# Kernel optimization log

Measured on AMD Instinct MI355X. Metric: run time of the kernel, lower is better.

Reference implementation:

```python
import jax, jax.numpy as jnp
import numpy as np

M, LAM, MAX_ITER, TOL, BETA = 5, 1e-4, 50, 0.01, 1.0


def anderson_fixed_point(lin_w, lin_b, x0):
    """Anderson acceleration for x = Linear(x), faithful to the torch loop.
    x0: (bsz, d, H, W); the fixed-point map applies the linear over W."""
    bsz = x0.shape[0]
    n = x0.size // bsz
    shape = x0.shape
    dt = x0.dtype

    def f(v_flat):  # (bsz, n) -> (bsz, n)
        return (v_flat.reshape(shape) @ lin_w.T + lin_b).reshape(bsz, n)

    x0f = x0.reshape(bsz, n)
    F0 = f(x0f)
    X = jnp.zeros((bsz, M, n), dt).at[:, 0].set(x0f).at[:, 1].set(F0)
    Fm = jnp.zeros((bsz, M, n), dt).at[:, 0].set(F0).at[:, 1].set(f(F0))
    y = jnp.zeros((bsz, M + 1), dt).at[:, 0].set(1.0)
    eyeM = jnp.eye(M, dtype=dt)

    def cond(c):
        _, _, k, res = c
        return (k < MAX_ITER) & (res >= TOL)

    def body(c):
        X, Fm, k, _ = c
        nk = jnp.minimum(k, M)
        # mask inactive history slots (k < M early iterations); padded rows/cols
        # get lam on the diagonal and 0 border -> alpha_j = 0 there, identical
        # to torch's solve on the leading (n+1)x(n+1) submatrix.
        mask = (jnp.arange(M) < nk).astype(dt)               # (M,)
        G = (Fm - X) * mask[None, :, None]                   # (bsz, M, n)
        Hin = jnp.einsum('bin,bjn->bij', G, G) + LAM * eyeM  # (bsz, M, M)
        H = jnp.zeros((bsz, M + 1, M + 1), dt)
        H = H.at[:, 0, 1:].set(mask).at[:, 1:, 0].set(mask).at[:, 1:, 1:].set(Hin)
        alpha = jnp.linalg.solve(H, y[..., None])[:, 1:, 0]  # (bsz, M)
        xnew = BETA * jnp.einsum('bm,bmn->bn', alpha, Fm) + (1.0 - BETA) * jnp.einsum('bm,bmn->bn', alpha, X)
        idx = k % M
        X = X.at[:, idx].set(xnew)
        fnew = f(xnew)
        Fm = Fm.at[:, idx].set(fnew)
        res = jnp.linalg.norm(fnew - xnew) / (1e-5 + jnp.linalg.norm(fnew))
        return (X, Fm, k + 1, res)

    Xf, _, kf, _ = jax.lax.while_loop(
        cond, body, (X, Fm, jnp.int32(2), jnp.asarray(jnp.inf, dt)))
    return Xf[:, (kf - 1) % M].reshape(shape)


def setup_inputs() -> dict:
    key = jax.random.key(0)
    k1, k2, k3, k4, k5 = jax.random.split(key, 5)
    B, D, H, W = 16, 8, 128, 512  # in_features = out_features = W = 512
    x = jax.random.normal(k1, (B, D, H, W), jnp.float32)
    # contractive inner linear so the fixed-point iteration behaves
    lin_w = jax.random.normal(k2, (W, W), jnp.float32) * 0.02
    lin_b = jax.random.normal(k3, (W,), jnp.float32) * 0.1
    weight = jax.random.normal(k4, (W, W), jnp.float32) * 0.02
    bias = jax.random.normal(k5, (W,), jnp.float32) * 0.1
    return {"x": x, "lin_w": lin_w, "lin_b": lin_b, "weight": weight, "bias": bias}


def reference(x, lin_w, lin_b, weight, bias):
    # torch runs the solver under no_grad -> stop_gradient for fidelity
    x_star = anderson_fixed_point(
        jax.lax.stop_gradient(lin_w),
        jax.lax.stop_gradient(lin_b),
        jax.lax.stop_gradient(x))
    return x_star @ weight.T + bias
```

## Files before the change

### kernel.cpp

```cpp
#include <hip/hip_runtime.h>
#include <math.h>

#define FD     512
#define NBATCH 16
#define NROWS  16384
#define ROWS   64
#define NBLK   (NROWS/ROWS)
#define TPB    1024
#define MM     5
#define LAMV   1e-4f
#define MAXIT  50
#define TOLV   0.01f
#define NTOT   8388608
#define PADW   520

typedef __attribute__((ext_vector_type(8))) short  short8;
typedef __attribute__((ext_vector_type(4))) short  short4v;
typedef __attribute__((ext_vector_type(4))) float  float4v;

__device__ unsigned short g_Fm[MM][NTOT];
__device__ unsigned short g_G [MM][NTOT];
__device__ unsigned short g_Wb [FD*FD];
__device__ unsigned short g_WbO[FD*FD];
__device__ float g_acc [MAXIT-2][NBATCH][8];
__device__ float g_acc0[NBATCH][8];
__device__ float g_alpha[8];
__device__ int   g_lastk;

static __device__ __forceinline__ unsigned short f2bf(float f) {
    unsigned u = __float_as_uint(f);
    u += 0x7fff + ((u >> 16) & 1);
    return (unsigned short)(u >> 16);
}
static __device__ __forceinline__ float bf2f(unsigned short s) {
    return __uint_as_float(((unsigned)s) << 16);
}

template<int MODE>
static __device__ __forceinline__ void mfma_gemm(const unsigned short* __restrict__ Wb,
                                                 const float* __restrict__ bvec,
                                                 const unsigned short* AsIn,
                                                 unsigned short* FsOut,
                                                 float* __restrict__ gout)
{
    const int lane = threadIdx.x & 63;
    const int wv   = threadIdx.x >> 6;
    const int lm   = lane & 15;
    const int quad = lane >> 4;
    float4v acc[4][2];
#pragma unroll
    for (int ct = 0; ct < 2; ct++) {
        const int c0 = wv*32 + ct*16 + quad*4;
#pragma unroll
        for (int r = 0; r < 4; r++) {
            const float b = bvec[c0 + r];
#pragma unroll
            for (int r16 = 0; r16 < 4; r16++) acc[r16][ct][r] = b;
        }
    }
#pragma unroll
    for (int q = 0; q < 4; q++) {
#pragma unroll
        for (int kb = 0; kb < 4; kb++) {
            const int ko = q*128 + kb*32 + quad*8;
            short8 bf[2];
#pragma unroll
            for (int ct = 0; ct < 2; ct++)
                bf[ct] = *(const short8*)(Wb + (wv*32 + ct*16 + lm)*FD + ko);
            short8 af[4];
#pragma unroll
            for (int r16 = 0; r16 < 4; r16++)
                af[r16] = *(const short8*)(AsIn + (r16*16 + lm)*PADW + ko);
#pragma unroll
            for (int r16 = 0; r16 < 4; r16++) {
                acc[r16][0] = __builtin_amdgcn_mfma_f32_16x16x32_bf16(bf[0], af[r16], acc[r16][0], 0,0,0);
                acc[r16][1] = __builtin_amdgcn_mfma_f32_16x16x32_bf16(bf[1], af[r16], acc[r16][1], 0,0,0);
            }
        }
    }
#pragma unroll
    for (int ct = 0; ct < 2; ct++) {
        const int c0 = wv*32 + ct*16 + quad*4;
#pragma unroll
        for (int r16 = 0; r16 < 4; r16++) {
            const int row = r16*16 + lm;
            if (MODE == 0) {
                short4v v;
#pragma unroll
                for (int r = 0; r < 4; r++) v[r] = (short)f2bf(acc[r16][ct][r]);
                *(short4v*)(FsOut + row*PADW + c0) = v;
            } else {
                float4 v;
                v.x = acc[r16][ct][0]; v.y = acc[r16][ct][1];
                v.z = acc[r16][ct][2]; v.w = acc[r16][ct][3];
                *(float4*)(gout + row*FD + c0) = v;
            }
        }
    }
}

static __device__ __forceinline__ void red6(const float vals[6], float (*redS)[8], float* accrow)
{
    const int lane = threadIdx.x & 63, wv = threadIdx.x >> 6;
#pragma unroll
    for (int j = 0; j < 6; j++) {
        float v = vals[j];
#pragma unroll
        for (int o = 32; o; o >>= 1) v += __shfl_down(v, o);
        if (lane == 0) redS[wv][j] = v;
    }
    __syncthreads();
    if (threadIdx.x < 6) {
        float s = 0.f;
#pragma unroll
        for (int w = 0; w < 16; w++) s += redS[w][threadIdx.x];
        atomicAdd(accrow + threadIdx.x, s);
    }
}

__global__ void __launch_bounds__(256) k_init0(const float* __restrict__ lin_w,
                                               const float* __restrict__ weight)
{
    const int i0 = blockIdx.x*256 + threadIdx.x, stride = gridDim.x*256;
    for (int i = i0; i < FD*FD; i += stride) {
        g_Wb [i] = f2bf(lin_w[i]);
        g_WbO[i] = f2bf(weight[i]);
    }
    float* a = &g_acc[0][0][0];
    for (int i = i0; i < (MAXIT-2)*NBATCH*8; i += stride) a[i] = 0.f;
    float* a0 = &g_acc0[0][0];
    for (int i = i0; i < NBATCH*8; i += stride) a0[i] = 0.f;
}

__global__ void __launch_bounds__(TPB, 4) k_init1(const float* __restrict__ x,
                                                  const float* __restrict__ lin_b)
{
    __shared__ __align__(16) unsigned short As[ROWS*PADW];
    __shared__ __align__(16) unsigned short Fs[ROWS*PADW];
    __shared__ float redS[16][8];
    const int tid = threadIdx.x;
    const int t = blockIdx.x, b = t >> 4;
    const int base = t * (ROWS*FD);

#pragma unroll
    for (int i = 0; i < 4; i++) {
        const int e = (i*TPB + tid) * 8;
        const float4 a0 = *(const float4*)(x + base + e);
        const float4 a1 = *(const float4*)(x + base + e + 4);
        short8 v;
        v[0]=f2bf(a0.x); v[1]=f2bf(a0.y); v[2]=f2bf(a0.z); v[3]=f2bf(a0.w);
        v[4]=f2bf(a1.x); v[5]=f2bf(a1.y); v[6]=f2bf(a1.z); v[7]=f2bf(a1.w);
        *(short8*)(As + (e>>9)*PADW + (e&511)) = v;
    }
    __syncthreads();
    mfma_gemm<0>(g_Wb, lin_b, As, Fs, nullptr);
    __syncthreads();
    float d00 = 0.f;
#pragma unroll
    for (int i = 0; i < 4; i++) {
        const int e = (i*TPB + tid) * 8;
        const int off = base + e, lo = (e>>9)*PADW + (e&511);
        const short8 fv = *(const short8*)(Fs + lo);
        const short8 xv = *(const short8*)(As + lo);
        short8 gv;
#pragma unroll
        for (int j = 0; j < 8; j++) {
            const float g = bf2f((unsigned short)fv[j]) - bf2f((unsigned short)xv[j]);
            gv[j] = (short)f2bf(g);
            d00 = fmaf(g, g, d00);
        }
        *(short8*)(&g_Fm[0][off]) = fv;
        *(short8*)(&g_G [0][off]) = gv;
    }
    __syncthreads();
    mfma_gemm<0>(g_Wb, lin_b, Fs, As, nullptr);
    __syncthreads();
    float d01 = 0.f, d11 = 0.f;
#pragma unroll
    for (int i = 0; i < 4; i++) {
        const int e = (i*TPB + tid) * 8;
        const int off = base + e, lo = (e>>9)*PADW + (e&511);
        const short8 f1 = *(const short8*)(As + lo);
        const short8 f0 = *(const short8*)(Fs + lo);
        const short8 g0 = *(const short8*)(&g_G[0][off]);
        short8 gv;
#pragma unroll
        for (int j = 0; j < 8; j++) {
            const float g = bf2f((unsigned short)f1[j]) - bf2f((unsigned short)f0[j]);
            gv[j] = (short)f2bf(g);
            d11 = fmaf(g, g, d11);
            d01 = fmaf(bf2f((unsigned short)g0[j]), g, d01);
        }
        *(short8*)(&g_Fm[1][off]) = f1;
        *(short8*)(&g_G [1][off]) = gv;
    }
    const float vals[6] = {d00, d01, d11, 0.f, 0.f, 0.f};
    red6(vals, redS, &g_acc0[b][0]);
}

__global__ void __launch_bounds__(TPB, 4) k_iter(const float* __restrict__ lin_b, int k)
{
    __shared__ __align__(16) unsigned short As[ROWS*PADW];
    __shared__ __align__(16) unsigned short Fs[ROWS*PADW];
    __shared__ float gramS[MM][MM];
    __shared__ float alphaS[MM];
    __shared__ float Hs[48];
    __shared__ float redS[16][8];
    __shared__ float gAs[MM][MM];
    __shared__ float ga0S[3];
    __shared__ float sres;

    const int tid = threadIdx.x;
    const int t = blockIdx.x, b = t >> 4;
    const int base = t * (ROWS*FD);
    const int it = k - 2, idx = k % MM, nk = (k < MM) ? k : MM;
    const int j0 = (k - 5 > 2) ? (k - 5) : 2;

    if (k > 2 && (tid >> 6) == 0) {
        float v = 0.f;
        if (tid < 32) {
            const int bb = tid & 15;
            const int jj = (tid < 16) ? ((k-1) % MM) : 5;
            v = g_acc[it-1][bb][jj];
        }
        v += __shfl_xor(v, 1); v += __shfl_xor(v, 2);
        v += __shfl_xor(v, 4); v += __shfl_xor(v, 8);
        const float num = __shfl(v, 0), den = __shfl(v, 16);
        if (tid == 0) sres = sqrtf(num) / (1e-5f + sqrtf(den));
    }
    if ((tid >> 6) == 1) {
        const int l = tid & 63;
        if (l < 25) {
            const int jj = j0 + l/5;
            if (jj < k) gAs[l/5][l%5] = g_acc[jj-2][b][l%5];
        } else if (l < 28) {
            ga0S[l-25] = g_acc0[b][l-25];
        }
    }
    __syncthreads();
    if (k > 2 && sres < TOLV) return;

    short8 pf0[MM], pf1[MM];
#pragma unroll
    for (int m = 0; m < MM; m++) if (m < nk) {
        pf0[m] = *(const short8*)(&g_Fm[m][base + (0*TPB + tid)*8]);
        pf1[m] = *(const short8*)(&g_Fm[m][base + (1*TPB + tid)*8]);
    }
    __builtin_amdgcn_sched_barrier(0);

    if (tid == 0) {
#pragma unroll
        for (int i = 0; i < MM; i++)
#pragma unroll
            for (int j = 0; j < MM; j++) gramS[i][j] = 0.f;
        gramS[0][0] = ga0S[0];
        gramS[0][1] = gramS[1][0] = ga0S[1];
        gramS[1][1] = ga0S[2];
        for (int j = j0; j < k; j++) {
            const int ij = j % MM, nkj = (j < MM) ? j : MM;
            for (int c = 0; c < MM; c++)
                if (c < nkj || c == ij) {
                    const float vv = gAs[j - j0][c];
                    gramS[ij][c] = vv; gramS[c][ij] = vv;
                }
        }
        float* H = Hs;
        for (int i = 0; i < 42; i++) H[i] = 0.f;
        for (int j = 0; j < nk; j++) { H[1+j] = 1.f; H[(1+j)*7] = 1.f; }
#pragma unroll
        for (int i = 0; i < MM; i++) H[(1+i)*7 + (1+i)] = LAMV;
        for (int i = 0; i < nk; i++)
            for (int j = 0; j < nk; j++)
                H[(1+i)*7 + (1+j)] = gramS[i][j] + (i == j ? LAMV : 0.f);
        H[6] = 1.f;
        for (int col = 0; col < 6; col++) {
            int p = col; float mx = fabsf(H[col*7+col]);
            for (int r2 = col+1; r2 < 6; r2++) {
                const float vv = fabsf(H[r2*7+col]);
                if (vv > mx) { mx = vv; p = r2; }
            }
            if (p != col)
                for (int j = col; j < 7; j++) { const float tt = H[col*7+j]; H[col*7+j] = H[p*7+j]; H[p*7+j] = tt; }
            const float piv = H[col*7+col];
            for (int r2 = col+1; r2 < 6; r2++) {
                const float fct = H[r2*7+col] / piv;
                for (int j = col+1; j < 7; j++) H[r2*7+j] -= fct * H[col*7+j];
            }
        }
        for (int r2 = 5; r2 >= 0; r2--) {
            float s = H[r2*7+6];
            for (int j = r2+1; j < 6; j++) s -= H[r2*7+j] * H[j*7+6];
            H[r2*7+6] = s / H[r2*7+r2];
        }
#pragma unroll
        for (int m = 0; m < MM; m++) alphaS[m] = H[(1+m)*7+6];
        if (t == 0) {
#pragma unroll
            for (int m = 0; m < MM; m++) g_alpha[m] = H[(1+m)*7+6];
            g_lastk = k;
        }
    }
    __syncthreads();

    float al[MM];
#pragma unroll
    for (int m = 0; m < MM; m++) al[m] = alphaS[m];

#pragma unroll
    for (int i = 0; i < 4; i++) {
        const int e = (i*TPB + tid) * 8;
        const int off = base + e;
        float s[8] = {0,0,0,0,0,0,0,0};
#pragma unroll
        for (int m = 0; m < MM; m++) if (m < nk) {
            short8 fm;
            if (i == 0)      fm = pf0[m];
            else if (i == 1) fm = pf1[m];
            else             fm = *(const short8*)(&g_Fm[m][off]);
#pragma unroll
            for (int j = 0; j < 8; j++)
                s[j] = fmaf(al[m], bf2f((unsigned short)fm[j]), s[j]);
        }
        short8 v;
#pragma unroll
        for (int j = 0; j < 8; j++) v[j] = (short)f2bf(s[j]);
        *(short8*)(As + (e>>9)*PADW + (e&511)) = v;
    }
    __syncthreads();
    mfma_gemm<0>(g_Wb, lin_b, As, Fs, nullptr);
    __syncthreads();
    float dv[6] = {0,0,0,0,0,0};
    float dself = 0.f;
#pragma unroll
    for (int i = 0; i < 4; i++) {
        const int e = (i*TPB + tid) * 8;
        const int off = base + e, lo = (e>>9)*PADW + (e&511);
        const short8 fv = *(const short8*)(Fs + lo);
        const short8 xv = *(const short8*)(As + lo);
        float gg[8]; short8 gv;
#pragma unroll
        for (int j = 0; j < 8; j++) {
            const float ff = bf2f((unsigned short)fv[j]);
            const float g  = ff - bf2f((unsigned short)xv[j]);
            gg[j] = g; gv[j] = (short)f2bf(g);
            dv[5] = fmaf(ff, ff, dv[5]);
            dself = fmaf(g, g, dself);
        }
        *(short8*)(&g_Fm[idx][off]) = fv;
        *(short8*)(&g_G [idx][off]) = gv;
#pragma unroll
        for (int js = 0; js < MM; js++) {
            if (js != idx && js < nk) {
                const short8 gj = *(const short8*)(&g_G[js][off]);
#pragma unroll
                for (int j = 0; j < 8; j++)
                    dv[js] = fmaf(gg[j], bf2f((unsigned short)gj[j]), dv[js]);
            }
        }
    }
    float vals[6];
#pragma unroll
    for (int j = 0; j < MM; j++) vals[j] = (j == idx) ? (dv[j] + dself) : dv[j];
    vals[5] = dv[5];
    red6(vals, redS, &g_acc[it][b][0]);
}

__global__ void __launch_bounds__(TPB, 4) k_final(const float* __restrict__ bias,
                                                  float* __restrict__ out)
{
    __shared__ __align__(16) unsigned short As[ROWS*PADW];
    __shared__ float alphaS[MM];
    __shared__ int   nkS;
    const int tid = threadIdx.x;
    const int base = blockIdx.x * (ROWS*FD);

    if (tid == 0) {
        const int lk = g_lastk;
        nkS = (lk < MM) ? lk : MM;
#pragma unroll
        for (int m = 0; m < MM; m++) alphaS[m] = g_alpha[m];
    }
    __syncthreads();
    const int nk = nkS;
    float al[MM];
#pragma unroll
    for (int m = 0; m < MM; m++) al[m] = alphaS[m];

#pragma unroll
    for (int i = 0; i < 4; i++) {
        const int e = (i*TPB + tid) * 8;
        const int off = base + e;
        float s[8] = {0,0,0,0,0,0,0,0};
#pragma unroll
        for (int m = 0; m < MM; m++) if (m < nk) {
            const short8 fm = *(const short8*)(&g_Fm[m][off]);
#pragma unroll
            for (int j = 0; j < 8; j++)
                s[j] = fmaf(al[m], bf2f((unsigned short)fm[j]), s[j]);
        }
        short8 v;
#pragma unroll
        for (int j = 0; j < 8; j++) v[j] = (short)f2bf(s[j]);
        *(short8*)(As + (e>>9)*PADW + (e&511)) = v;
    }
    __syncthreads();
    mfma_gemm<1>(g_WbO, bias, As, nullptr, out + base);
}

extern "C" void kernel_launch(void* const* d_in, const int* in_sizes, int n_in,
                              void* d_out, int out_size, void* d_ws, size_t ws_size,
                              hipStream_t stream)
{
    (void)in_sizes; (void)n_in; (void)out_size; (void)d_ws; (void)ws_size;
    const float* x      = (const float*)d_in[0];
    const float* lin_w  = (const float*)d_in[1];
    const float* lin_b  = (const float*)d_in[2];
    const float* weight = (const float*)d_in[3];
    const float* bias   = (const float*)d_in[4];
    float* out = (float*)d_out;

    hipLaunchKernelGGL(k_init0, dim3(512),  dim3(256), 0, stream, lin_w, weight);
    hipLaunchKernelGGL(k_init1, dim3(NBLK), dim3(TPB), 0, stream, x, lin_b);
    for (int k = 2; k < MAXIT; k++)
        hipLaunchKernelGGL(k_iter, dim3(NBLK), dim3(TPB), 0, stream, lin_b, k);
    hipLaunchKernelGGL(k_final, dim3(NBLK), dim3(TPB), 0, stream, bias, out);
}
```

Before: 630.7 us.

## Halve rows per block, compute GEMM in place in one LDS buffer

Each block now handles 32 rows instead of 64, so the grid doubles. The separate Fs shared buffer is dropped: the MFMA GEMM writes its result back into As between two barriers, and the x and F values are kept in registers. The early-exit residual check is now done by every wave with no shared variable or barrier. The Fm prefetch before the alpha solve is removed, and k_init1 recomputes G0 rather than re-reading it. Together this cuts LDS use per block, aiming for higher occupancy (launch bounds raised to 8), at the cost of more blocks each re-reading the whole weight matrix and extra barriers inside the GEMM.

Result: slower. 764.5 us (+21.2%).

```diff
diff --git a/kernel.cpp b/kernel.cpp
--- a/kernel.cpp
+++ b/kernel.cpp
@@ -4,9 +4,10 @@
 #define FD     512
 #define NBATCH 16
 #define NROWS  16384
-#define ROWS   64
+#define ROWS   32
 #define NBLK   (NROWS/ROWS)
 #define TPB    1024
+#define BPB    32
 #define MM     5
 #define LAMV   1e-4f
 #define MAXIT  50
@@ -37,17 +38,16 @@
 }
 
 template<int MODE>
-static __device__ __forceinline__ void mfma_gemm(const unsigned short* __restrict__ Wb,
-                                                 const float* __restrict__ bvec,
-                                                 const unsigned short* AsIn,
-                                                 unsigned short* FsOut,
-                                                 float* __restrict__ gout)
+static __device__ __forceinline__ void mfma_ip(const unsigned short* __restrict__ Wb,
+                                               const float* __restrict__ bvec,
+                                               unsigned short* As,
+                                               float* __restrict__ gout)
 {
     const int lane = threadIdx.x & 63;
     const int wv   = threadIdx.x >> 6;
     const int lm   = lane & 15;
     const int quad = lane >> 4;
-    float4v acc[4][2];
+    float4v acc[2][2];
 #pragma unroll
     for (int ct = 0; ct < 2; ct++) {
         const int c0 = wv*32 + ct*16 + quad*4;
@@ -55,7 +55,7 @@
         for (int r = 0; r < 4; r++) {
             const float b = bvec[c0 + r];
 #pragma unroll
-            for (int r16 = 0; r16 < 4; r16++) acc[r16][ct][r] = b;
+            for (int r16 = 0; r16 < 2; r16++) acc[r16][ct][r] = b;
         }
     }
 #pragma unroll
@@ -67,28 +67,29 @@
 #pragma unroll
             for (int ct = 0; ct < 2; ct++)
                 bf[ct] = *(const short8*)(Wb + (wv*32 + ct*16 + lm)*FD + ko);
-            short8 af[4];
-#pragma unroll
-            for (int r16 = 0; r16 < 4; r16++)
-                af[r16] = *(const short8*)(AsIn + (r16*16 + lm)*PADW + ko);
-#pragma unroll
-            for (int r16 = 0; r16 < 4; r16++) {
+            short8 af[2];
+#pragma unroll
+            for (int r16 = 0; r16 < 2; r16++)
+                af[r16] = *(const short8*)(As + (r16*16 + lm)*PADW + ko);
+#pragma unroll
+            for (int r16 = 0; r16 < 2; r16++) {
                 acc[r16][0] = __builtin_amdgcn_mfma_f32_16x16x32_bf16(bf[0], af[r16], acc[r16][0], 0,0,0);
                 acc[r16][1] = __builtin_amdgcn_mfma_f32_16x16x32_bf16(bf[1], af[r16], acc[r16][1], 0,0,0);
             }
         }
     }
+    if (MODE == 0) __syncthreads();
 #pragma unroll
     for (int ct = 0; ct < 2; ct++) {
         const int c0 = wv*32 + ct*16 + quad*4;
 #pragma unroll
-        for (int r16 = 0; r16 < 4; r16++) {
+        for (int r16 = 0; r16 < 2; r16++) {
             const int row = r16*16 + lm;
             if (MODE == 0) {
                 short4v v;
 #pragma unroll
                 for (int r = 0; r < 4; r++) v[r] = (short)f2bf(acc[r16][ct][r]);
-                *(short4v*)(FsOut + row*PADW + c0) = v;
+                *(short4v*)(As + row*PADW + c0) = v;
             } else {
                 float4 v;
                 v.x = acc[r16][ct][0]; v.y = acc[r16][ct][1];
@@ -97,6 +98,7 @@
             }
         }
     }
+    if (MODE == 0) __syncthreads();
 }
 
 static __device__ __forceinline__ void red6(const float vals[6], float (*redS)[8], float* accrow)
@@ -132,36 +134,37 @@
     for (int i = i0; i < NBATCH*8; i += stride) a0[i] = 0.f;
 }
 
-__global__ void __launch_bounds__(TPB, 4) k_init1(const float* __restrict__ x,
+__global__ void __launch_bounds__(TPB, 8) k_init1(const float* __restrict__ x,
                                                   const float* __restrict__ lin_b)
 {
     __shared__ __align__(16) unsigned short As[ROWS*PADW];
-    __shared__ __align__(16) unsigned short Fs[ROWS*PADW];
     __shared__ float redS[16][8];
     const int tid = threadIdx.x;
-    const int t = blockIdx.x, b = t >> 4;
+    const int t = blockIdx.x, b = t >> 5;
     const int base = t * (ROWS*FD);
 
-#pragma unroll
-    for (int i = 0; i < 4; i++) {
+    short8 xh[2];
+#pragma unroll
+    for (int i = 0; i < 2; i++) {
         const int e = (i*TPB + tid) * 8;
         const float4 a0 = *(const float4*)(x + base + e);
         const float4 a1 = *(const float4*)(x + base + e + 4);
         short8 v;
         v[0]=f2bf(a0.x); v[1]=f2bf(a0.y); v[2]=f2bf(a0.z); v[3]=f2bf(a0.w);
         v[4]=f2bf(a1.x); v[5]=f2bf(a1.y); v[6]=f2bf(a1.z); v[7]=f2bf(a1.w);
+        xh[i] = v;
         *(short8*)(As + (e>>9)*PADW + (e&511)) = v;
     }
     __syncthreads();
-    mfma_gemm<0>(g_Wb, lin_b, As, Fs, nullptr);
-    __syncthreads();
+    mfma_ip<0>(g_Wb, lin_b, As, nullptr);
     float d00 = 0.f;
-#pragma unroll
-    for (int i = 0; i < 4; i++) {
+    short8 fh[2];
+#pragma unroll
+    for (int i = 0; i < 2; i++) {
         const int e = (i*TPB + tid) * 8;
         const int off = base + e, lo = (e>>9)*PADW + (e&511);
-        const short8 fv = *(const short8*)(Fs + lo);
-        const short8 xv = *(const short8*)(As + lo);
+        const short8 fv = *(const short8*)(As + lo);
+        const short8 xv = xh[i];
         short8 gv;
 #pragma unroll
         for (int j = 0; j < 8; j++) {
@@ -171,25 +174,25 @@
         }
         *(short8*)(&g_Fm[0][off]) = fv;
         *(short8*)(&g_G [0][off]) = gv;
-    }
-    __syncthreads();
-    mfma_gemm<0>(g_Wb, lin_b, Fs, As, nullptr);
-    __syncthreads();
+        fh[i] = fv;
+    }
+    mfma_ip<0>(g_Wb, lin_b, As, nullptr);
     float d01 = 0.f, d11 = 0.f;
 #pragma unroll
-    for (int i = 0; i < 4; i++) {
+    for (int i = 0; i < 2; i++) {
         const int e = (i*TPB + tid) * 8;
         const int off = base + e, lo = (e>>9)*PADW + (e&511);
         const short8 f1 = *(const short8*)(As + lo);
-        const short8 f0 = *(const short8*)(Fs + lo);
-        const short8 g0 = *(const short8*)(&g_G[0][off]);
+        const short8 f0 = fh[i];
+        const short8 xv = xh[i];
         short8 gv;
 #pragma unroll
         for (int j = 0; j < 8; j++) {
             const float g = bf2f((unsigned short)f1[j]) - bf2f((unsigned short)f0[j]);
             gv[j] = (short)f2bf(g);
             d11 = fmaf(g, g, d11);
-            d01 = fmaf(bf2f((unsigned short)g0[j]), g, d01);
+            const float g0 = bf2f(f2bf(bf2f((unsigned short)f0[j]) - bf2f((unsigned short)xv[j])));
+            d01 = fmaf(g0, g, d01);
         }
         *(short8*)(&g_Fm[1][off]) = f1;
         *(short8*)(&g_G [1][off]) = gv;
@@ -198,36 +201,36 @@
     red6(vals, redS, &g_acc0[b][0]);
 }
 
-__global__ void __launch_bounds__(TPB, 4) k_iter(const float* __restrict__ lin_b, int k)
+__global__ void __launch_bounds__(TPB, 8) k_iter(const float* __restrict__ lin_b, int k)
 {
     __shared__ __align__(16) unsigned short As[ROWS*PADW];
-    __shared__ __align__(16) unsigned short Fs[ROWS*PADW];
     __shared__ float gramS[MM][MM];
     __shared__ float alphaS[MM];
     __shared__ float Hs[48];
     __shared__ float redS[16][8];
     __shared__ float gAs[MM][MM];
     __shared__ float ga0S[3];
-    __shared__ float sres;
-
     const int tid = threadIdx.x;
-    const int t = blockIdx.x, b = t >> 4;
+    const int t = blockIdx.x, b = t >> 5;
     const int base = t * (ROWS*FD);
     const int it = k - 2, idx = k % MM, nk = (k < MM) ? k : MM;
     const int j0 = (k - 5 > 2) ? (k - 5) : 2;
 
-    if (k > 2 && (tid >> 6) == 0) {
+    if (k > 2) {
         float v = 0.f;
-        if (tid < 32) {
-            const int bb = tid & 15;
-            const int jj = (tid < 16) ? ((k-1) % MM) : 5;
+        const int l = tid & 63;
+        if (l < 32) {
+            const int bb = l & 15;
+            const int jj = (l < 16) ? ((k-1) % MM) : 5;
             v = g_acc[it-1][bb][jj];
         }
         v += __shfl_xor(v, 1); v += __shfl_xor(v, 2);
         v += __shfl_xor(v, 4); v += __shfl_xor(v, 8);
         const float num = __shfl(v, 0), den = __shfl(v, 16);
-        if (tid == 0) sres = sqrtf(num) / (1e-5f + sqrtf(den));
-    }
+        const float sres = sqrtf(num) / (1e-5f + sqrtf(den));
+        if (sres < TOLV) return;
+    }
+
     if ((tid >> 6) == 1) {
         const int l = tid & 63;
         if (l < 25) {
@@ -238,15 +241,6 @@
         }
     }
     __syncthreads();
-    if (k > 2 && sres < TOLV) return;
-
-    short8 pf0[MM], pf1[MM];
-#pragma unroll
-    for (int m = 0; m < MM; m++) if (m < nk) {
-        pf0[m] = *(const short8*)(&g_Fm[m][base + (0*TPB + tid)*8]);
-        pf1[m] = *(const short8*)(&g_Fm[m][base + (1*TPB + tid)*8]);
-    }
-    __builtin_amdgcn_sched_barrier(0);
 
     if (tid == 0) {
 #pragma unroll
@@ -306,17 +300,15 @@
 #pragma unroll
     for (int m = 0; m < MM; m++) al[m] = alphaS[m];
 
-#pragma unroll
-    for (int i = 0; i < 4; i++) {
+    short8 xh[2];
+#pragma unroll
+    for (int i = 0; i < 2; i++) {
         const int e = (i*TPB + tid) * 8;
         const int off = base + e;
         float s[8] = {0,0,0,0,0,0,0,0};
 #pragma unroll
         for (int m = 0; m < MM; m++) if (m < nk) {
-            short8 fm;
-            if (i == 0)      fm = pf0[m];
-            else if (i == 1) fm = pf1[m];
-            else             fm = *(const short8*)(&g_Fm[m][off]);
+            const short8 fm = *(const short8*)(&g_Fm[m][off]);
 #pragma unroll
             for (int j = 0; j < 8; j++)
                 s[j] = fmaf(al[m], bf2f((unsigned short)fm[j]), s[j]);
@@ -324,19 +316,19 @@
         short8 v;
 #pragma unroll
         for (int j = 0; j < 8; j++) v[j] = (short)f2bf(s[j]);
+        xh[i] = v;
         *(short8*)(As + (e>>9)*PADW + (e&511)) = v;
     }
     __syncthreads();
-    mfma_gemm<0>(g_Wb, lin_b, As, Fs, nullptr);
-    __syncthreads();
+    mfma_ip<0>(g_Wb, lin_b, As, nullptr);
     float dv[6] = {0,0,0,0,0,0};
     float dself = 0.f;
 #pragma unroll
-    for (int i = 0; i < 4; i++) {
+    for (int i = 0; i < 2; i++) {
         const int e = (i*TPB + tid) * 8;
         const int off = base + e, lo = (e>>9)*PADW + (e&511);
-        const short8 fv = *(const short8*)(Fs + lo);
-        const short8 xv = *(const short8*)(As + lo);
+        const short8 fv = *(const short8*)(As + lo);
+        const short8 xv = xh[i];
         float gg[8]; short8 gv;
 #pragma unroll
         for (int j = 0; j < 8; j++) {
@@ -365,7 +357,7 @@
     red6(vals, redS, &g_acc[it][b][0]);
 }
 
-__global__ void __launch_bounds__(TPB, 4) k_final(const float* __restrict__ bias,
+__global__ void __launch_bounds__(TPB, 8) k_final(const float* __restrict__ bias,
                                                   float* __restrict__ out)
 {
     __shared__ __align__(16) unsigned short As[ROWS*PADW];
@@ -387,7 +379,7 @@
     for (int m = 0; m < MM; m++) al[m] = alphaS[m];
 
 #pragma unroll
-    for (int i = 0; i < 4; i++) {
+    for (int i = 0; i < 2; i++) {
         const int e = (i*TPB + tid) * 8;
         const int off = base + e;
         float s[8] = {0,0,0,0,0,0,0,0};
@@ -404,7 +396,7 @@
         *(short8*)(As + (e>>9)*PADW + (e&511)) = v;
     }
     __syncthreads();
-    mfma_gemm<1>(g_WbO, bias, As, nullptr, out + base);
+    mfma_ip<1>(g_WbO, bias, As, out + base);
 }
 
 extern "C" void kernel_launch(void* const* d_in, const int* in_sizes, int n_in,
```
